# Optimization experiments

Measured on AMD Instinct MI355X. Metric: run time of the kernel, lower is better.

Reference implementation:

```python
import jax, jax.numpy as jnp
import numpy as np

DEPTH, DIM, HEADS, DIM_HEAD, MLP = 6, 768, 12, 64, 3072
INNER = HEADS * DIM_HEAD  # 768
EPS = 1e-5


def _layernorm(x, w, b):
    m = jnp.mean(x, axis=-1, keepdims=True)
    v = jnp.mean((x - m) ** 2, axis=-1, keepdims=True)
    return (x - m) * jax.lax.rsqrt(v + EPS) * w + b


def setup_inputs() -> dict:
    key = jax.random.key(0)
    ks = jax.random.split(key, 12)
    s = 0.02
    return {
        "x": jax.random.normal(ks[0], (4, 1024, DIM), dtype=jnp.float32),
        "ln1_w": jnp.ones((DEPTH, DIM), jnp.float32),
        "ln1_b": jnp.zeros((DEPTH, DIM), jnp.float32),
        "w_qkv": jax.random.normal(ks[1], (DEPTH, DIM, 3 * INNER), jnp.float32) * s,
        "w_o": jax.random.normal(ks[2], (DEPTH, INNER, DIM), jnp.float32) * s,
        "b_o": jnp.zeros((DEPTH, DIM), jnp.float32),
        "ln2_w": jnp.ones((DEPTH, DIM), jnp.float32),
        "ln2_b": jnp.zeros((DEPTH, DIM), jnp.float32),
        "w1": jax.random.normal(ks[3], (DEPTH, DIM, MLP), jnp.float32) * s,
        "b1": jnp.zeros((DEPTH, MLP), jnp.float32),
        "w2": jax.random.normal(ks[4], (DEPTH, MLP, DIM), jnp.float32) * s,
        "b2": jnp.zeros((DEPTH, DIM), jnp.float32),
    }


def _forward(x, ln1_w, ln1_b, w_qkv, w_o, b_o, ln2_w, ln2_b, w1, b1, w2, b2):
    scale = DIM_HEAD ** -0.5
    b, n, _ = x.shape

    def block(x, p):
        l1w, l1b, wqkv, wo, bo, l2w, l2b, W1, B1, W2, B2 = p
        # --- attention (pre-norm); dropout/droppath are identity in eval ---
        h = _layernorm(x, l1w, l1b)
        qkv = h @ wqkv                                   # [b, n, 3*inner]
        q, k, v = jnp.split(qkv, 3, axis=-1)
        q = q.reshape(b, n, HEADS, DIM_HEAD).transpose(0, 2, 1, 3)
        k = k.reshape(b, n, HEADS, DIM_HEAD).transpose(0, 2, 1, 3)
        v = v.reshape(b, n, HEADS, DIM_HEAD).transpose(0, 2, 1, 3)
        dots = jnp.einsum('bhid,bhjd->bhij', q, k) * scale   # [b, h, n, n]
        attn = jax.nn.softmax(dots, axis=-1)
        out = jnp.einsum('bhij,bhjd->bhid', attn, v)
        out = out.transpose(0, 2, 1, 3).reshape(b, n, INNER)
        x = x + out @ wo + bo
        # --- feed-forward (pre-norm), exact GELU like torch default ---
        h = _layernorm(x, l2w, l2b)
        x = x + jax.nn.gelu(h @ W1 + B1, approximate=False) @ W2 + B2
        return x, None

    x, _ = jax.lax.scan(block, x, (ln1_w, ln1_b, w_qkv, w_o, b_o,
                                   ln2_w, ln2_b, w1, b1, w2, b2))
    return x


def reference(x, ln1_w, ln1_b, w_qkv, w_o, b_o, ln2_w, ln2_b, w1, b1, w2, b2):
    return _forward(x, ln1_w, ln1_b, w_qkv, w_o, b_o, ln2_w, ln2_b, w1, b1, w2, b2)
```

## Files before the change

kernel.cpp:

```cpp
#include <hip/hip_runtime.h>
#include <cmath>
#include <cstdint>

typedef __bf16 bf16_t;
typedef __bf16 bf16x8 __attribute__((ext_vector_type(8)));
typedef __bf16 bf16x4 __attribute__((ext_vector_type(4)));
typedef float  f32x4  __attribute__((ext_vector_type(4)));

#define DEPTH 6
#define DIM   768
#define HEADS 12
#define DH    64
#define MLPD  3072
#define SEQ   1024
#define BATCH 4
#define MTOT  (BATCH*SEQ)
#define QKVN  2304

static __device__ __forceinline__ bf16x8 ld8(const bf16_t* p) {
    return *(const bf16x8*)p;
}

typedef const __attribute__((address_space(1))) unsigned int gas_u32;
typedef __attribute__((address_space(3))) unsigned int las_u32;
static __device__ __forceinline__ void gload16(const bf16_t* g, bf16_t* l) {
    __builtin_amdgcn_global_load_lds((gas_u32*)g, (las_u32*)l, 16, 0, 0);
}

__global__ __launch_bounds__(256) void tcvt_kernel(const float* __restrict__ in,
                                                   bf16_t* __restrict__ out,
                                                   int K, int N) {
    __shared__ float ts[32][33];
    int n0 = blockIdx.x * 32, k0 = blockIdx.y * 32;
    size_t base = (size_t)blockIdx.z * K * N;
    int tx = threadIdx.x & 31, ty = threadIdx.x >> 5;
    #pragma unroll
    for (int r = 0; r < 32; r += 8)
        ts[ty + r][tx] = in[base + (size_t)(k0 + ty + r) * N + n0 + tx];
    __syncthreads();
    #pragma unroll
    for (int r = 0; r < 32; r += 8)
        out[base + (size_t)(n0 + ty + r) * K + k0 + tx] = (bf16_t)ts[tx][ty + r];
}

__global__ __launch_bounds__(256) void ln_kernel(const float* __restrict__ x,
                                                 const float* __restrict__ w,
                                                 const float* __restrict__ b,
                                                 bf16_t* __restrict__ h) {
    int row = blockIdx.x, t = threadIdx.x;
    const float* xr = x + (size_t)row * DIM;
    float v0 = xr[t], v1 = xr[t + 256], v2 = xr[t + 512];
    float s = v0 + v1 + v2;
    float q = v0 * v0 + v1 * v1 + v2 * v2;
    #pragma unroll
    for (int off = 32; off > 0; off >>= 1) {
        s += __shfl_down(s, off);
        q += __shfl_down(q, off);
    }
    __shared__ float ss[4], sq[4], stat[2];
    if ((t & 63) == 0) { ss[t >> 6] = s; sq[t >> 6] = q; }
    __syncthreads();
    if (t == 0) {
        float S = ss[0] + ss[1] + ss[2] + ss[3];
        float Q = sq[0] + sq[1] + sq[2] + sq[3];
        float mean = S * (1.0f / DIM);
        float var  = Q * (1.0f / DIM) - mean * mean;
        stat[0] = mean;
        stat[1] = rsqrtf(var + 1e-5f);
    }
    __syncthreads();
    float mean = stat[0], rstd = stat[1];
    bf16_t* hr = h + (size_t)row * DIM;
    hr[t]       = (bf16_t)((v0 - mean) * rstd * w[t]       + b[t]);
    hr[t + 256] = (bf16_t)((v1 - mean) * rstd * w[t + 256] + b[t + 256]);
    hr[t + 512] = (bf16_t)((v2 - mean) * rstd * w[t + 512] + b[t + 512]);
}

template <int EPI>
__global__ __launch_bounds__(256) void gemm_kernel(const bf16_t* __restrict__ A,
                                                   const bf16_t* __restrict__ Bt,
                                                   const float* __restrict__ bias,
                                                   bf16_t* __restrict__ Cb,
                                                   float* __restrict__ Cf,
                                                   int N, int K, int klen) {
    __shared__ __align__(16) bf16_t As[128 * 32];
    __shared__ __align__(16) bf16_t Bs[128 * 32];
    int t = threadIdx.x;
    int m0 = blockIdx.y * 128, n0 = blockIdx.x * 128;
    int kz = blockIdx.z;
    int kbeg = kz * klen, kend = kbeg + klen;
    int lane = t & 63, l16 = lane & 15, quad = lane >> 4;
    int wv = t >> 6, wm = wv >> 1, wn = wv & 1;
    f32x4 acc[4][4] = {};

    int srow = wv * 16 + (lane >> 2);
    int skc  = (lane & 3) * 8;
    const bf16_t* ga0 = A  + (size_t)(m0 + srow) * K + skc;
    const bf16_t* ga1 = ga0 + (size_t)64 * K;
    const bf16_t* gb0 = Bt + (size_t)(n0 + srow) * K + skc;
    const bf16_t* gb1 = gb0 + (size_t)64 * K;
    bf16_t* la0 = &As[(wv * 16) * 32];
    bf16_t* la1 = &As[(64 + wv * 16) * 32];
    bf16_t* lb0 = &Bs[(wv * 16) * 32];
    bf16_t* lb1 = &Bs[(64 + wv * 16) * 32];

    for (int k0 = kbeg; k0 < kend; k0 += 32) {
        __syncthreads();
        gload16(ga0 + k0, la0);
        gload16(ga1 + k0, la1);
        gload16(gb0 + k0, lb0);
        gload16(gb1 + k0, lb1);
        __syncthreads();
        bf16x8 af[4], bfr[4];
        #pragma unroll
        for (int i = 0; i < 4; i++)
            af[i] = ld8(&As[(wm * 64 + i * 16 + l16) * 32 + quad * 8]);
        #pragma unroll
        for (int j = 0; j < 4; j++)
            bfr[j] = ld8(&Bs[(wn * 64 + j * 16 + l16) * 32 + quad * 8]);
        #pragma unroll
        for (int i = 0; i < 4; i++)
            #pragma unroll
            for (int j = 0; j < 4; j++)
                acc[i][j] = __builtin_amdgcn_mfma_f32_16x16x32_bf16(af[i], bfr[j], acc[i][j], 0, 0, 0);
    }

    #pragma unroll
    for (int i = 0; i < 4; i++) {
        int grow = m0 + wm * 64 + i * 16 + quad * 4;
        #pragma unroll
        for (int j = 0; j < 4; j++) {
            int gcol = n0 + wn * 64 + j * 16 + l16;
            float bv = 0.0f;
            if constexpr (EPI != 0) bv = bias[gcol];
            #pragma unroll
            for (int r = 0; r < 4; r++) {
                size_t idx = (size_t)(grow + r) * N + gcol;
                float v = acc[i][j][r];
                if constexpr (EPI == 0) {
                    Cb[idx] = (bf16_t)v;
                } else if constexpr (EPI == 1) {
                    v += bv;
                    v = 0.5f * v * (1.0f + erff(v * 0.70710678118654752f));
                    Cb[idx] = (bf16_t)v;
                } else {
                    float add = v + (blockIdx.z == 0 ? bv : 0.0f);
                    atomicAdd(&Cf[idx], add);
                }
            }
        }
    }
}

__global__ __launch_bounds__(256) void vtrans_kernel(const bf16_t* __restrict__ qkv,
                                                     bf16_t* __restrict__ vt) {
    int nt = blockIdx.x;
    int bh = blockIdx.y;
    int b = bh / HEADS, h = bh % HEADS;
    __shared__ bf16_t ts[64 * 65];
    int t = threadIdx.x;
    #pragma unroll
    for (int s = 0; s < 16; s++) {
        int flat = s * 256 + t;
        int r = flat >> 6, d = flat & 63;
        ts[d * 65 + r] = qkv[((size_t)(b * SEQ) + nt * 64 + r) * QKVN + 1536 + h * 64 + d];
    }
    __syncthreads();
    #pragma unroll
    for (int s = 0; s < 16; s++) {
        int flat = s * 256 + t;
        int d = flat >> 6, c = flat & 63;
        vt[((size_t)bh * 64 + d) * SEQ + nt * 64 + c] = ts[d * 65 + c];
    }
}

__global__ __launch_bounds__(256) void attn_kernel(const bf16_t* __restrict__ qkv,
                                                   const bf16_t* __restrict__ vt,
                                                   bf16_t* __restrict__ out) {
    int qt = blockIdx.x, h = blockIdx.y, b = blockIdx.z;
    int t = threadIdx.x;
    int wv = t >> 6, lane = t & 63, l16 = lane & 15, quad = lane >> 4;
    const float LOG2E = 1.44269504f;
    int qw0 = qt * 64 + wv * 16;

    __shared__ __align__(16) bf16_t Ks[2][64 * 32];
    __shared__ __align__(16) bf16_t Vs[64 * 64];
    __shared__ __align__(16) bf16_t Pa[4][16 * 72];
    bf16_t* P = Pa[wv];

    size_t bS = (size_t)b * SEQ;
    const bf16_t* qrow = qkv + (bS + qw0 + l16) * QKVN + h * 64;
    bf16x8 qf0 = ld8(qrow + quad * 8);
    bf16x8 qf1 = ld8(qrow + 32 + quad * 8);

    float m = -3e38f, l = 0.0f;
    f32x4 o[4] = {};

    const bf16_t* kbase = qkv + bS * QKVN + 768 + h * 64;
    const bf16_t* vbase = vt + ((size_t)(b * HEADS + h) * 64) * SEQ;

    for (int kb = 0; kb < SEQ; kb += 64) {
        __syncthreads();
        if (wv < 2) {
            #pragma unroll
            for (int j = 0; j < 4; j++) {
                int i = wv * 4 + j, p = i & 1, rg = i >> 1;
                gload16(kbase + (size_t)(kb + rg * 16 + (lane >> 2)) * QKVN
                              + p * 32 + (lane & 3) * 8,
                        &Ks[p][rg * 16 * 32]);
            }
        } else {
            #pragma unroll
            for (int j = 0; j < 4; j++) {
                int dg = (wv - 2) * 4 + j;
                gload16(vbase + (size_t)(dg * 8 + (lane >> 3)) * SEQ
                              + kb + (lane & 7) * 8,
                        &Vs[dg * 8 * 64]);
            }
        }
        __syncthreads();

        f32x4 s[4];
        #pragma unroll
        for (int tt = 0; tt < 4; tt++) {
            f32x4 z = {};
            z = __builtin_amdgcn_mfma_f32_16x16x32_bf16(
                    ld8(&Ks[0][(tt * 16 + l16) * 32 + quad * 8]), qf0, z, 0, 0, 0);
            z = __builtin_amdgcn_mfma_f32_16x16x32_bf16(
                    ld8(&Ks[1][(tt * 16 + l16) * 32 + quad * 8]), qf1, z, 0, 0, 0);
            s[tt] = z;
        }
        float mx = -3e38f;
        #pragma unroll
        for (int tt = 0; tt < 4; tt++)
            #pragma unroll
            for (int r = 0; r < 4; r++) {
                s[tt][r] *= 0.125f;
                mx = fmaxf(mx, s[tt][r]);
            }
        mx = fmaxf(mx, __shfl_xor(mx, 16));
        mx = fmaxf(mx, __shfl_xor(mx, 32));
        float mn = fmaxf(m, mx);
        float alpha = exp2f((m - mn) * LOG2E);
        m = mn;
        float nb = mn * LOG2E;
        float rs = 0.0f;
        #pragma unroll
        for (int tt = 0; tt < 4; tt++) {
            bf16x4 pkt;
            #pragma unroll
            for (int r = 0; r < 4; r++) {
                float p = exp2f(fmaf(s[tt][r], LOG2E, -nb));
                rs += p;
                pkt[r] = (bf16_t)p;
            }
            *(bf16x4*)&P[l16 * 72 + tt * 16 + quad * 4] = pkt;
        }
        l = l * alpha + rs;
        #pragma unroll
        for (int jt = 0; jt < 4; jt++) o[jt] *= alpha;
        asm volatile("s_waitcnt lgkmcnt(0)" ::: "memory");
        bf16x8 pf0 = ld8(&P[l16 * 72 + quad * 8]);
        bf16x8 pf1 = ld8(&P[l16 * 72 + 32 + quad * 8]);
        #pragma unroll
        for (int jt = 0; jt < 4; jt++) {
            const bf16_t* vp = &Vs[(jt * 16 + l16) * 64];
            o[jt] = __builtin_amdgcn_mfma_f32_16x16x32_bf16(ld8(vp + quad * 8), pf0, o[jt], 0, 0, 0);
            o[jt] = __builtin_amdgcn_mfma_f32_16x16x32_bf16(ld8(vp + 32 + quad * 8), pf1, o[jt], 0, 0, 0);
        }
    }

    l += __shfl_xor(l, 16);
    l += __shfl_xor(l, 32);
    float inv = 1.0f / l;
    bf16_t* orow = out + (bS + qw0 + l16) * DIM + h * 64;
    #pragma unroll
    for (int jt = 0; jt < 4; jt++) {
        bf16x4 ov;
        #pragma unroll
        for (int r = 0; r < 4; r++) ov[r] = (bf16_t)(o[jt][r] * inv);
        *(bf16x4*)&orow[jt * 16 + quad * 4] = ov;
    }
}

extern "C" void kernel_launch(void* const* d_in, const int* in_sizes, int n_in,
                              void* d_out, int out_size, void* d_ws, size_t ws_size,
                              hipStream_t stream) {
    const float* x     = (const float*)d_in[0];
    const float* ln1_w = (const float*)d_in[1];
    const float* ln1_b = (const float*)d_in[2];
    const float* w_qkv = (const float*)d_in[3];
    const float* w_o   = (const float*)d_in[4];
    const float* b_o   = (const float*)d_in[5];
    const float* ln2_w = (const float*)d_in[6];
    const float* ln2_b = (const float*)d_in[7];
    const float* w1    = (const float*)d_in[8];
    const float* b1    = (const float*)d_in[9];
    const float* w2    = (const float*)d_in[10];
    const float* b2    = (const float*)d_in[11];
    float* out = (float*)d_out;

    char* ws = (char*)d_ws;
    size_t off = 0;
    auto alloc = [&](size_t elems) -> bf16_t* {
        bf16_t* p = (bf16_t*)(ws + off);
        off += (elems * 2 + 255) & ~(size_t)255;
        return p;
    };
    bf16_t* wqkv_t = alloc((size_t)DEPTH * DIM * QKVN);
    bf16_t* wo_t   = alloc((size_t)DEPTH * DIM * DIM);
    bf16_t* w1_t   = alloc((size_t)DEPTH * DIM * MLPD);
    bf16_t* w2_t   = alloc((size_t)DEPTH * MLPD * DIM);
    bf16_t* hbuf   = alloc((size_t)MTOT * DIM);
    bf16_t* qkvb   = alloc((size_t)MTOT * QKVN);
    bf16_t* vtb    = alloc((size_t)BATCH * HEADS * 64 * SEQ);
    bf16_t* aob    = alloc((size_t)MTOT * DIM);
    bf16_t* midb   = alloc((size_t)MTOT * MLPD);
    if (off > ws_size) return;

    tcvt_kernel<<<dim3(QKVN / 32, DIM / 32, DEPTH), 256, 0, stream>>>(w_qkv, wqkv_t, DIM, QKVN);
    tcvt_kernel<<<dim3(DIM / 32,  DIM / 32, DEPTH), 256, 0, stream>>>(w_o,   wo_t,   DIM, DIM);
    tcvt_kernel<<<dim3(MLPD / 32, DIM / 32, DEPTH), 256, 0, stream>>>(w1,    w1_t,   DIM, MLPD);
    tcvt_kernel<<<dim3(DIM / 32, MLPD / 32, DEPTH), 256, 0, stream>>>(w2,    w2_t,   MLPD, DIM);

    hipMemcpyAsync(out, x, (size_t)MTOT * DIM * 4, hipMemcpyDeviceToDevice, stream);

    for (int L = 0; L < DEPTH; L++) {
        ln_kernel<<<MTOT, 256, 0, stream>>>(out, ln1_w + L * DIM, ln1_b + L * DIM, hbuf);
        gemm_kernel<0><<<dim3(QKVN / 128, MTOT / 128, 1), 256, 0, stream>>>(
            hbuf, wqkv_t + (size_t)L * DIM * QKVN, nullptr, qkvb, nullptr, QKVN, DIM, DIM);
        vtrans_kernel<<<dim3(16, BATCH * HEADS), 256, 0, stream>>>(qkvb, vtb);
        attn_kernel<<<dim3(SEQ / 64, HEADS, BATCH), 256, 0, stream>>>(qkvb, vtb, aob);
        gemm_kernel<2><<<dim3(DIM / 128, MTOT / 128, 2), 256, 0, stream>>>(
            aob, wo_t + (size_t)L * DIM * DIM, b_o + L * DIM, nullptr, out, DIM, DIM, 384);
        ln_kernel<<<MTOT, 256, 0, stream>>>(out, ln2_w + L * DIM, ln2_b + L * DIM, hbuf);
        gemm_kernel<1><<<dim3(MLPD / 128, MTOT / 128, 1), 256, 0, stream>>>(
            hbuf, w1_t + (size_t)L * DIM * MLPD, b1 + L * MLPD, midb, nullptr, MLPD, DIM, DIM);
        gemm_kernel<2><<<dim3(DIM / 128, MTOT / 128, 4), 256, 0, stream>>>(
            midb, w2_t + (size_t)L * MLPD * DIM, b2 + L * DIM, nullptr, out, DIM, MLPD, 768);
    }
}
```

Measured before the change: 1.505 ms.

## Replace atomic split-K with partial buffers reduced inside fused residual+LayerNorm

Split-K GEMMs now write per-slice fp32 partials to workspace instead of doing atomicAdd into the residual. A new LN kernel sums the partials, adds the bias and residual, writes the residual and emits the next LayerNorm in one pass. The V transpose is folded into the QKV GEMM epilogue, and the GEMM main loop stages 64 K per sync. This removes atomics and the separate vtrans launch but adds extra fp32 partial traffic and reuses the qkv buffer as scratch.

```diff
diff --git a/kernel.cpp b/kernel.cpp
--- a/kernel.cpp
+++ b/kernel.cpp
@@ -43,15 +43,35 @@
         out[base + (size_t)(n0 + ty + r) * K + k0 + tx] = (bf16_t)ts[tx][ty + r];
 }
 
-__global__ __launch_bounds__(256) void ln_kernel(const float* __restrict__ x,
-                                                 const float* __restrict__ w,
-                                                 const float* __restrict__ b,
-                                                 bf16_t* __restrict__ h) {
+__global__ __launch_bounds__(256) void lnr_kernel(const float* __restrict__ xin,
+                                                  float* __restrict__ xout,
+                                                  const float* __restrict__ P,
+                                                  int nslices,
+                                                  const float* __restrict__ bias,
+                                                  const float* __restrict__ w,
+                                                  const float* __restrict__ b,
+                                                  bf16_t* __restrict__ h,
+                                                  int writeLN) {
     int row = blockIdx.x, t = threadIdx.x;
-    const float* xr = x + (size_t)row * DIM;
-    float v0 = xr[t], v1 = xr[t + 256], v2 = xr[t + 512];
-    float s = v0 + v1 + v2;
-    float q = v0 * v0 + v1 * v1 + v2 * v2;
+    size_t ro = (size_t)row * DIM;
+    float v[3];
+    #pragma unroll
+    for (int e = 0; e < 3; e++) {
+        int c = t + e * 256;
+        float xv = xin[ro + c];
+        if (nslices) {
+            xv += bias[c];
+            for (int s = 0; s < nslices; s++)
+                xv += P[(size_t)s * MTOT * DIM + ro + c];
+        }
+        v[e] = xv;
+    }
+    if (nslices) {
+        #pragma unroll
+        for (int e = 0; e < 3; e++) xout[ro + t + e * 256] = v[e];
+    }
+    float s = v[0] + v[1] + v[2];
+    float q = v[0] * v[0] + v[1] * v[1] + v[2] * v[2];
     #pragma unroll
     for (int off = 32; off > 0; off >>= 1) {
         s += __shfl_down(s, off);
@@ -69,11 +89,14 @@
         stat[1] = rsqrtf(var + 1e-5f);
     }
     __syncthreads();
-    float mean = stat[0], rstd = stat[1];
-    bf16_t* hr = h + (size_t)row * DIM;
-    hr[t]       = (bf16_t)((v0 - mean) * rstd * w[t]       + b[t]);
-    hr[t + 256] = (bf16_t)((v1 - mean) * rstd * w[t + 256] + b[t + 256]);
-    hr[t + 512] = (bf16_t)((v2 - mean) * rstd * w[t + 512] + b[t + 512]);
+    if (writeLN) {
+        float mean = stat[0], rstd = stat[1];
+        #pragma unroll
+        for (int e = 0; e < 3; e++) {
+            int c = t + e * 256;
+            h[ro + c] = (bf16_t)((v[e] - mean) * rstd * w[c] + b[c]);
+        }
+    }
 }
 
 template <int EPI>
@@ -82,9 +105,10 @@
                                                    const float* __restrict__ bias,
                                                    bf16_t* __restrict__ Cb,
                                                    float* __restrict__ Cf,
+                                                   bf16_t* __restrict__ Vt,
                                                    int N, int K, int klen) {
-    __shared__ __align__(16) bf16_t As[128 * 32];
-    __shared__ __align__(16) bf16_t Bs[128 * 32];
+    __shared__ __align__(16) bf16_t As[2][128 * 32];
+    __shared__ __align__(16) bf16_t Bs[2][128 * 32];
     int t = threadIdx.x;
     int m0 = blockIdx.y * 128, n0 = blockIdx.x * 128;
     int kz = blockIdx.z;
@@ -95,36 +119,56 @@
 
     int srow = wv * 16 + (lane >> 2);
     int skc  = (lane & 3) * 8;
-    const bf16_t* ga0 = A  + (size_t)(m0 + srow) * K + skc;
-    const bf16_t* ga1 = ga0 + (size_t)64 * K;
-    const bf16_t* gb0 = Bt + (size_t)(n0 + srow) * K + skc;
-    const bf16_t* gb1 = gb0 + (size_t)64 * K;
-    bf16_t* la0 = &As[(wv * 16) * 32];
-    bf16_t* la1 = &As[(64 + wv * 16) * 32];
-    bf16_t* lb0 = &Bs[(wv * 16) * 32];
-    bf16_t* lb1 = &Bs[(64 + wv * 16) * 32];
-
-    for (int k0 = kbeg; k0 < kend; k0 += 32) {
+    const bf16_t* ga = A  + (size_t)(m0 + srow) * K + skc;
+    const bf16_t* gb = Bt + (size_t)(n0 + srow) * K + skc;
+    size_t rh = (size_t)64 * K;
+
+    for (int k0 = kbeg; k0 < kend; k0 += 64) {
         __syncthreads();
-        gload16(ga0 + k0, la0);
-        gload16(ga1 + k0, la1);
-        gload16(gb0 + k0, lb0);
-        gload16(gb1 + k0, lb1);
+        #pragma unroll
+        for (int p = 0; p < 2; p++) {
+            gload16(ga + k0 + p * 32,      &As[p][(wv * 16) * 32]);
+            gload16(ga + rh + k0 + p * 32, &As[p][(64 + wv * 16) * 32]);
+            gload16(gb + k0 + p * 32,      &Bs[p][(wv * 16) * 32]);
+            gload16(gb + rh + k0 + p * 32, &Bs[p][(64 + wv * 16) * 32]);
+        }
         __syncthreads();
-        bf16x8 af[4], bfr[4];
-        #pragma unroll
-        for (int i = 0; i < 4; i++)
-            af[i] = ld8(&As[(wm * 64 + i * 16 + l16) * 32 + quad * 8]);
-        #pragma unroll
-        for (int j = 0; j < 4; j++)
-            bfr[j] = ld8(&Bs[(wn * 64 + j * 16 + l16) * 32 + quad * 8]);
-        #pragma unroll
-        for (int i = 0; i < 4; i++)
+        #pragma unroll
+        for (int p = 0; p < 2; p++) {
+            bf16x8 af[4], bfr[4];
+            #pragma unroll
+            for (int i = 0; i < 4; i++)
+                af[i] = ld8(&As[p][(wm * 64 + i * 16 + l16) * 32 + quad * 8]);
             #pragma unroll
             for (int j = 0; j < 4; j++)
-                acc[i][j] = __builtin_amdgcn_mfma_f32_16x16x32_bf16(af[i], bfr[j], acc[i][j], 0, 0, 0);
-    }
-
+                bfr[j] = ld8(&Bs[p][(wn * 64 + j * 16 + l16) * 32 + quad * 8]);
+            #pragma unroll
+            for (int i = 0; i < 4; i++)
+                #pragma unroll
+                for (int j = 0; j < 4; j++)
+                    acc[i][j] = __builtin_amdgcn_mfma_f32_16x16x32_bf16(af[i], bfr[j], acc[i][j], 0, 0, 0);
+        }
+    }
+
+    if constexpr (EPI == 0) {
+        if (n0 >= 1536) {
+            int b = m0 >> 10;
+            #pragma unroll
+            for (int i = 0; i < 4; i++) {
+                int n = (m0 & 1023) + wm * 64 + i * 16 + quad * 4;
+                #pragma unroll
+                for (int j = 0; j < 4; j++) {
+                    int hc = n0 + wn * 64 + j * 16 + l16 - 1536;
+                    int hh = hc >> 6, d = hc & 63;
+                    bf16x4 ov;
+                    #pragma unroll
+                    for (int r = 0; r < 4; r++) ov[r] = (bf16_t)acc[i][j][r];
+                    *(bf16x4*)&Vt[(((size_t)b * HEADS + hh) * 64 + d) * SEQ + n] = ov;
+                }
+            }
+            return;
+        }
+    }
     #pragma unroll
     for (int i = 0; i < 4; i++) {
         int grow = m0 + wm * 64 + i * 16 + quad * 4;
@@ -132,7 +176,7 @@
         for (int j = 0; j < 4; j++) {
             int gcol = n0 + wn * 64 + j * 16 + l16;
             float bv = 0.0f;
-            if constexpr (EPI != 0) bv = bias[gcol];
+            if constexpr (EPI == 1) bv = bias[gcol];
             #pragma unroll
             for (int r = 0; r < 4; r++) {
                 size_t idx = (size_t)(grow + r) * N + gcol;
@@ -144,33 +188,10 @@
                     v = 0.5f * v * (1.0f + erff(v * 0.70710678118654752f));
                     Cb[idx] = (bf16_t)v;
                 } else {
-                    float add = v + (blockIdx.z == 0 ? bv : 0.0f);
-                    atomicAdd(&Cf[idx], add);
+                    Cf[(size_t)kz * MTOT * N + idx] = v;
                 }
             }
         }
-    }
-}
-
-__global__ __launch_bounds__(256) void vtrans_kernel(const bf16_t* __restrict__ qkv,
-                                                     bf16_t* __restrict__ vt) {
-    int nt = blockIdx.x;
-    int bh = blockIdx.y;
-    int b = bh / HEADS, h = bh % HEADS;
-    __shared__ bf16_t ts[64 * 65];
-    int t = threadIdx.x;
-    #pragma unroll
-    for (int s = 0; s < 16; s++) {
-        int flat = s * 256 + t;
-        int r = flat >> 6, d = flat & 63;
-        ts[d * 65 + r] = qkv[((size_t)(b * SEQ) + nt * 64 + r) * QKVN + 1536 + h * 64 + d];
-    }
-    __syncthreads();
-    #pragma unroll
-    for (int s = 0; s < 16; s++) {
-        int flat = s * 256 + t;
-        int d = flat >> 6, c = flat & 63;
-        vt[((size_t)bh * 64 + d) * SEQ + nt * 64 + c] = ts[d * 65 + c];
     }
 }
 
@@ -302,20 +323,22 @@
 
     char* ws = (char*)d_ws;
     size_t off = 0;
-    auto alloc = [&](size_t elems) -> bf16_t* {
-        bf16_t* p = (bf16_t*)(ws + off);
-        off += (elems * 2 + 255) & ~(size_t)255;
+    auto alloc = [&](size_t bytes) -> char* {
+        char* p = ws + off;
+        off += (bytes + 255) & ~(size_t)255;
         return p;
     };
-    bf16_t* wqkv_t = alloc((size_t)DEPTH * DIM * QKVN);
-    bf16_t* wo_t   = alloc((size_t)DEPTH * DIM * DIM);
-    bf16_t* w1_t   = alloc((size_t)DEPTH * DIM * MLPD);
-    bf16_t* w2_t   = alloc((size_t)DEPTH * MLPD * DIM);
-    bf16_t* hbuf   = alloc((size_t)MTOT * DIM);
-    bf16_t* qkvb   = alloc((size_t)MTOT * QKVN);
-    bf16_t* vtb    = alloc((size_t)BATCH * HEADS * 64 * SEQ);
-    bf16_t* aob    = alloc((size_t)MTOT * DIM);
-    bf16_t* midb   = alloc((size_t)MTOT * MLPD);
+    bf16_t* wqkv_t = (bf16_t*)alloc((size_t)DEPTH * DIM * QKVN * 2);
+    bf16_t* wo_t   = (bf16_t*)alloc((size_t)DEPTH * DIM * DIM * 2);
+    bf16_t* w1_t   = (bf16_t*)alloc((size_t)DEPTH * DIM * MLPD * 2);
+    bf16_t* w2_t   = (bf16_t*)alloc((size_t)DEPTH * MLPD * DIM * 2);
+    bf16_t* hbuf   = (bf16_t*)alloc((size_t)MTOT * DIM * 2);
+    bf16_t* qkvb   = (bf16_t*)alloc((size_t)MTOT * QKVN * 2);
+    bf16_t* vtb    = (bf16_t*)alloc((size_t)BATCH * HEADS * 64 * SEQ * 2);
+    bf16_t* aob    = (bf16_t*)alloc((size_t)MTOT * DIM * 2);
+    bf16_t* midb   = (bf16_t*)alloc((size_t)MTOT * MLPD * 2);
+    float*  Pm     = (float*)alloc((size_t)4 * MTOT * DIM * 4);
+    float*  Pp     = (float*)qkvb;
     if (off > ws_size) return;
 
     tcvt_kernel<<<dim3(QKVN / 32, DIM / 32, DEPTH), 256, 0, stream>>>(w_qkv, wqkv_t, DIM, QKVN);
@@ -325,18 +348,32 @@
 
     hipMemcpyAsync(out, x, (size_t)MTOT * DIM * 4, hipMemcpyDeviceToDevice, stream);
 
+    lnr_kernel<<<MTOT, 256, 0, stream>>>(out, out, nullptr, 0, nullptr,
+                                         ln1_w, ln1_b, hbuf, 1);
+
     for (int L = 0; L < DEPTH; L++) {
-        ln_kernel<<<MTOT, 256, 0, stream>>>(out, ln1_w + L * DIM, ln1_b + L * DIM, hbuf);
         gemm_kernel<0><<<dim3(QKVN / 128, MTOT / 128, 1), 256, 0, stream>>>(
-            hbuf, wqkv_t + (size_t)L * DIM * QKVN, nullptr, qkvb, nullptr, QKVN, DIM, DIM);
-        vtrans_kernel<<<dim3(16, BATCH * HEADS), 256, 0, stream>>>(qkvb, vtb);
+            hbuf, wqkv_t + (size_t)L * DIM * QKVN, nullptr, qkvb, nullptr, vtb,
+            QKVN, DIM, DIM);
         attn_kernel<<<dim3(SEQ / 64, HEADS, BATCH), 256, 0, stream>>>(qkvb, vtb, aob);
         gemm_kernel<2><<<dim3(DIM / 128, MTOT / 128, 2), 256, 0, stream>>>(
-            aob, wo_t + (size_t)L * DIM * DIM, b_o + L * DIM, nullptr, out, DIM, DIM, 384);
-        ln_kernel<<<MTOT, 256, 0, stream>>>(out, ln2_w + L * DIM, ln2_b + L * DIM, hbuf);
+            aob, wo_t + (size_t)L * DIM * DIM, nullptr, nullptr, Pp, nullptr,
+            DIM, DIM, 384);
+        lnr_kernel<<<MTOT, 256, 0, stream>>>(out, out, Pp, 2, b_o + L * DIM,
+                                             ln2_w + L * DIM, ln2_b + L * DIM, hbuf, 1);
         gemm_kernel<1><<<dim3(MLPD / 128, MTOT / 128, 1), 256, 0, stream>>>(
-            hbuf, w1_t + (size_t)L * DIM * MLPD, b1 + L * MLPD, midb, nullptr, MLPD, DIM, DIM);
+            hbuf, w1_t + (size_t)L * DIM * MLPD, b1 + L * MLPD, midb, nullptr, nullptr,
+            MLPD, DIM, DIM);
         gemm_kernel<2><<<dim3(DIM / 128, MTOT / 128, 4), 256, 0, stream>>>(
-            midb, w2_t + (size_t)L * MLPD * DIM, b2 + L * DIM, nullptr, out, DIM, MLPD, 768);
-    }
-}
+            midb, w2_t + (size_t)L * MLPD * DIM, nullptr, nullptr, Pm, nullptr,
+            DIM, MLPD, 768);
+        if (L < DEPTH - 1) {
+            lnr_kernel<<<MTOT, 256, 0, stream>>>(out, out, Pm, 4, b2 + L * DIM,
+                                                 ln1_w + (L + 1) * DIM,
+                                                 ln1_b + (L + 1) * DIM, hbuf, 1);
+        } else {
+            lnr_kernel<<<MTOT, 256, 0, stream>>>(out, out, Pm, 4, b2 + L * DIM,
+                                                 ln1_w, ln1_b, hbuf, 0);
+        }
+    }
+}
```

New measurement: 1.346 ms. -10.6%, faster.
